# Kernel tuning notes

Hardware: AMD Instinct MI355X
Metric: run time of the kernel (lower is better)

The kernel has to match this reference:

```python
import jax, jax.numpy as jnp
import numpy as np

N, E, D, L, R = 100000, 500000, 128, 2, 10
EPS = 1e-5  # BatchNorm1d default eps


def setup_inputs() -> dict:
    key = jax.random.key(0)
    ks = jax.random.split(key, 10)
    return {
        "in_node_emb": jax.random.normal(ks[0], (N, D), jnp.float32),
        "in_rel_emb": jax.random.normal(ks[1], (R, D), jnp.float32),
        "w_in": jax.random.normal(ks[2], (L, D, D), jnp.float32) * 0.05,
        "w_out": jax.random.normal(ks[3], (L, D, D), jnp.float32) * 0.05,
        "w_loop": jax.random.normal(ks[4], (L, D, D), jnp.float32) * 0.05,
        "w_rel": jax.random.normal(ks[5], (L, D, D), jnp.float32) * 0.05,
        "loop_rel": jax.random.normal(ks[6], (L, 1, D), jnp.float32) * 0.05,
        "bias": jnp.zeros((L, D), jnp.float32),
        "edge_src": jax.random.randint(ks[7], (E,), 0, N),
        "edge_dst": jax.random.randint(ks[8], (E,), 0, N),
        "edge_type": jax.random.randint(ks[9], (E,), 0, R),
    }


def _gcn_forward(in_node_emb, in_rel_emb, w_in, w_out, w_loop, w_rel, loop_rel,
                 bias, edge_src, edge_dst, edge_type):
    x, r = in_node_emb, in_rel_emb
    ones_e = jnp.ones((E,), in_node_emb.dtype)
    for l in range(L):
        rel = jnp.concatenate([r, loop_rel[l]], axis=0)  # [R+1, D]; last row = self-loop relation
        rel_e = rel[edge_type]                            # [E, D] per-edge relation embedding

        def directed_msg(row, col, w):
            # gather -> compose ('mult') -> linear -> degree norm -> scatter-add at row
            comp = x[col] * rel_e                         # [E, D]
            m = comp @ w                                  # [E, D]
            deg = jnp.zeros((N,), x.dtype).at[row].add(ones_e)
            dinv = jnp.where(deg > 0, jax.lax.rsqrt(deg), 0.0)
            m = m * (dinv[row] * dinv[col])[:, None]
            return jnp.zeros((N, D), x.dtype).at[row].add(m)

        in_res = directed_msg(edge_src, edge_dst, w_in[l])   # original direction (src<-dst msgs)
        out_res = directed_msg(edge_dst, edge_src, w_out[l]) # mirrored direction
        loop_res = (x * loop_rel[l]) @ w_loop[l]             # self-loop (no norm)
        out = (in_res + out_res + loop_res) * (1.0 / 3.0) + bias[l]
        # BatchNorm1d over nodes, batch statistics, gamma=1 beta=0
        mean = out.mean(axis=0)
        var = out.var(axis=0)
        out = (out - mean) * jax.lax.rsqrt(var + EPS)
        x = jnp.tanh(out)
        r = (rel @ w_rel[l])[:-1]                            # transform rels, drop loop row
    return x, r


def reference(in_node_emb, in_rel_emb, w_in, w_out, w_loop, w_rel, loop_rel,
              bias, edge_src, edge_dst, edge_type):
    return _gcn_forward(in_node_emb, in_rel_emb, w_in, w_out, w_loop, w_rel,
                        loop_rel, bias, edge_src, edge_dst, edge_type)
```

## Files before the change

kernel.cpp:

```cpp
#include <hip/hip_runtime.h>
#include <math.h>

#define Nn 100000
#define Ee 500000
#define Dd 128
#define Rr 10
#define ND (Nn * Dd)
#define SCAN_CHUNK 1024
#define NBLK ((Nn + SCAN_CHUNK - 1) / SCAN_CHUNK)
#define LDK 136
#define EPSF 1e-5f

typedef _Float16 half_t;
typedef __attribute__((ext_vector_type(8))) _Float16 half8;
typedef __attribute__((ext_vector_type(4))) float f32x4;
typedef unsigned short ushort;
typedef unsigned int uint;
typedef unsigned long long u64;

union H2 { uint u; _Float16 h[2]; };
union H4 { u64 u; _Float16 h[4]; };
union H8 { uint4 q; _Float16 h[8]; };

__device__ __forceinline__ void atomAddF(float* p, float v) {
    unsafeAtomicAdd(p, v);
}

__global__ void kzeroi(int* p, int n) {
    int i = blockIdx.x * blockDim.x + threadIdx.x;
    int stride = gridDim.x * blockDim.x;
    for (; i < n; i += stride) p[i] = 0;
}

__global__ void khist(const int* __restrict__ src, const int* __restrict__ dst,
                      int* cnt_s, int* cnt_d, int ne) {
    int e = blockIdx.x * blockDim.x + threadIdx.x;
    if (e < ne) {
        atomicAdd(&cnt_s[src[e]], 1);
        atomicAdd(&cnt_d[dst[e]], 1);
    }
}

__global__ __launch_bounds__(256) void kscan1(
    const int* __restrict__ cnt_s, const int* __restrict__ cnt_d,
    int* off_s, int* off_d, int* bsum_s, int* bsum_d,
    float* dinv_s, float* dinv_d) {
    int dir = blockIdx.x >= NBLK;
    int lb = blockIdx.x - dir * NBLK;
    const int* cnt = dir ? cnt_d : cnt_s;
    int* off = dir ? off_d : off_s;
    int* bsum = dir ? bsum_d : bsum_s;
    float* dinv = dir ? dinv_d : dinv_s;
    __shared__ int s[256];
    int tid = threadIdx.x;
    int base = lb * SCAN_CHUNK + tid * 4;
    int v[4], sum = 0;
#pragma unroll
    for (int q = 0; q < 4; q++) {
        int c = (base + q < Nn) ? cnt[base + q] : 0;
        v[q] = c;
        sum += c;
        if (base + q < Nn) dinv[base + q] = (c > 0) ? rsqrtf((float)c) : 0.f;
    }
    s[tid] = sum;
    __syncthreads();
#pragma unroll
    for (int ofs = 1; ofs < 256; ofs <<= 1) {
        int t = (tid >= ofs) ? s[tid - ofs] : 0;
        __syncthreads();
        s[tid] += t;
        __syncthreads();
    }
    if (tid == 255) bsum[lb] = s[255];
    int run = s[tid] - sum;
#pragma unroll
    for (int q = 0; q < 4; q++) {
        if (base + q < Nn) off[base + q] = run;
        run += v[q];
    }
}

__global__ __launch_bounds__(128) void kscan2(int* bsum_s, int* bsum_d,
                                              int* off_s, int* off_d) {
    int dir = blockIdx.x;
    int* bsum = dir ? bsum_d : bsum_s;
    int* off = dir ? off_d : off_s;
    __shared__ int s[128];
    int tid = threadIdx.x;
    int v = (tid < NBLK) ? bsum[tid] : 0;
    s[tid] = v;
    __syncthreads();
#pragma unroll
    for (int ofs = 1; ofs < 128; ofs <<= 1) {
        int t = (tid >= ofs) ? s[tid - ofs] : 0;
        __syncthreads();
        s[tid] += t;
        __syncthreads();
    }
    if (tid < NBLK) bsum[tid] = s[tid] - v;
    if (tid == 127) off[Nn] = s[127];
}

__global__ void kscan3(int* off_s, int* off_d, const int* __restrict__ bsum_s,
                       const int* __restrict__ bsum_d, int* cur_s, int* cur_d) {
    int idx = blockIdx.x * blockDim.x + threadIdx.x;
    if (idx >= 2 * Nn) return;
    int dir = idx >= Nn;
    int i = idx - dir * Nn;
    int* off = dir ? off_d : off_s;
    const int* bsum = dir ? bsum_d : bsum_s;
    int* cur = dir ? cur_d : cur_s;
    int o = off[i] + bsum[i >> 10];
    off[i] = o;
    cur[i] = o;
}

__global__ void kscatter(const int* __restrict__ src, const int* __restrict__ dst,
                         const int* __restrict__ typ,
                         const float* __restrict__ dinv_s, const float* __restrict__ dinv_d,
                         int* cur_s, int* cur_d,
                         int* pack_s, float* norm_s, int* pack_d, float* norm_d, int ne) {
    int e = blockIdx.x * blockDim.x + threadIdx.x;
    if (e >= ne) return;
    int s = src[e], d = dst[e], t = typ[e];
    int ps = atomicAdd(&cur_s[s], 1);
    pack_s[ps] = (d << 4) | t;
    norm_s[ps] = dinv_s[s] * dinv_s[d];
    int pd = atomicAdd(&cur_d[d], 1);
    pack_d[pd] = (s << 4) | t;
    norm_d[pd] = dinv_d[d] * dinv_d[s];
}

__global__ __launch_bounds__(256) void kprep(
    const float* __restrict__ x, const float* __restrict__ lr0,
    const float* __restrict__ w_in, const float* __restrict__ w_out,
    const float* __restrict__ w_loop, const float* __restrict__ w_rel,
    const float* __restrict__ r0,
    half_t* __restrict__ xb, half_t* __restrict__ xlb,
    half_t* __restrict__ Wt, float* __restrict__ r1, float* __restrict__ r2) {
    int blk = blockIdx.x;
    int tid = threadIdx.x;
    if (blk < ND / 8 / 256) {
        int idx = blk * 256 + tid;
        int base = idx * 8;
        int k = base & 127;
        float4 v0 = *(const float4*)(x + base);
        float4 v1 = *(const float4*)(x + base + 4);
        float4 l0 = *(const float4*)(lr0 + k);
        float4 l1 = *(const float4*)(lr0 + k + 4);
        H8 xo, xl;
        xo.h[0] = (half_t)v0.x; xo.h[1] = (half_t)v0.y; xo.h[2] = (half_t)v0.z; xo.h[3] = (half_t)v0.w;
        xo.h[4] = (half_t)v1.x; xo.h[5] = (half_t)v1.y; xo.h[6] = (half_t)v1.z; xo.h[7] = (half_t)v1.w;
        xl.h[0] = (half_t)(v0.x * l0.x); xl.h[1] = (half_t)(v0.y * l0.y);
        xl.h[2] = (half_t)(v0.z * l0.z); xl.h[3] = (half_t)(v0.w * l0.w);
        xl.h[4] = (half_t)(v1.x * l1.x); xl.h[5] = (half_t)(v1.y * l1.y);
        xl.h[6] = (half_t)(v1.z * l1.z); xl.h[7] = (half_t)(v1.w * l1.w);
        *(uint4*)(xb + base) = xo.q;
        *(uint4*)(xlb + base) = xl.q;
    } else if (blk < ND / 8 / 256 + 384) {
        int idx = (blk - ND / 8 / 256) * 256 + tid;
        int l = idx >= 49152;
        int rem = idx - l * 49152;
        int p = rem >> 14, r2i = rem & 16383;
        int n = r2i >> 7, k = r2i & 127;
        const float* W = (p == 0) ? (w_in + l * 16384)
                       : ((p == 1) ? (w_out + l * 16384) : (w_loop + l * 16384));
        Wt[idx] = (half_t)W[k * 128 + n];
    } else {
        __shared__ float sr[Rr * Dd];
        for (int i = tid; i < Rr * Dd; i += 256) sr[i] = r0[i];
        __syncthreads();
        for (int ph = 0; ph < 2; ph++) {
            const float* w = w_rel + ph * 16384;
            float o[5];
#pragma unroll
            for (int q = 0; q < 5; q++) {
                int oi = tid + q * 256;
                int row = oi >> 7, j = oi & 127;
                float acc = 0.f;
                for (int k = 0; k < 128; k++) acc += sr[row * 128 + k] * w[k * 128 + j];
                o[q] = acc;
            }
            __syncthreads();
            float* dst = ph ? r2 : r1;
#pragma unroll
            for (int q = 0; q < 5; q++) {
                int oi = tid + q * 256;
                sr[oi] = o[q];
                dst[oi] = o[q];
            }
            __syncthreads();
        }
    }
}

__global__ __launch_bounds__(256) void kgather(
    const int* __restrict__ off_s, const int* __restrict__ pack_s, const float* __restrict__ nrm_s,
    const int* __restrict__ off_d, const int* __restrict__ pack_d, const float* __restrict__ nrm_d,
    const half_t* __restrict__ xb, const float* __restrict__ rel,
    half_t* __restrict__ aggin, half_t* __restrict__ aggout, int gb) {
    int blk = blockIdx.x;
    const int *off, *pack; const float* nrm; half_t* agg;
    if (blk < gb) { off = off_s; pack = pack_s; nrm = nrm_s; agg = aggin; }
    else { blk -= gb; off = off_d; pack = pack_d; nrm = nrm_d; agg = aggout; }
    int wv = threadIdx.x >> 6;
    int lane = threadIdx.x & 63;
    int half = lane >> 5;
    int hl = lane & 31;
    int node = blk * 8 + wv * 2 + half;
    bool valid = node < Nn;
    int nodec = valid ? node : (Nn - 1);
    int b = off[nodec];
    int e = off[nodec + 1];
    int n_it = valid ? (e - b) : 0;
    int other = __shfl(n_it, lane ^ 32, 64);
    int mx = n_it > other ? n_it : other;

    const u64* x4 = (const u64*)xb;
    const float4* r4 = (const float4*)rel;
    float a0 = 0.f, a1 = 0.f, a2 = 0.f, a3 = 0.f;

    int it = 0;
    for (; it + 1 < mx; it += 2) {
        bool c0 = it < n_it, c1 = it + 1 < n_it;
        int i0 = c0 ? (b + it) : 0;
        int i1 = c1 ? (b + it + 1) : 0;
        int p0 = pack[i0], p1 = pack[i1];
        float w0 = c0 ? nrm[i0] : 0.f;
        float w1 = c1 ? nrm[i1] : 0.f;
        H4 xv0, xv1;
        xv0.u = x4[(size_t)(p0 >> 4) * 32 + hl];
        xv1.u = x4[(size_t)(p1 >> 4) * 32 + hl];
        float4 rv0 = r4[(p0 & 15) * 32 + hl];
        float4 rv1 = r4[(p1 & 15) * 32 + hl];
        a0 += (float)xv0.h[0] * rv0.x * w0;
        a1 += (float)xv0.h[1] * rv0.y * w0;
        a2 += (float)xv0.h[2] * rv0.z * w0;
        a3 += (float)xv0.h[3] * rv0.w * w0;
        a0 += (float)xv1.h[0] * rv1.x * w1;
        a1 += (float)xv1.h[1] * rv1.y * w1;
        a2 += (float)xv1.h[2] * rv1.z * w1;
        a3 += (float)xv1.h[3] * rv1.w * w1;
    }
    if (it < mx) {
        bool c0 = it < n_it;
        int i0 = c0 ? (b + it) : 0;
        int p0 = pack[i0];
        float w0 = c0 ? nrm[i0] : 0.f;
        H4 xv0; xv0.u = x4[(size_t)(p0 >> 4) * 32 + hl];
        float4 rv0 = r4[(p0 & 15) * 32 + hl];
        a0 += (float)xv0.h[0] * rv0.x * w0;
        a1 += (float)xv0.h[1] * rv0.y * w0;
        a2 += (float)xv0.h[2] * rv0.z * w0;
        a3 += (float)xv0.h[3] * rv0.w * w0;
    }
    if (valid) {
        H4 o;
        o.h[0] = (half_t)a0; o.h[1] = (half_t)a1;
        o.h[2] = (half_t)a2; o.h[3] = (half_t)a3;
        ((u64*)agg)[(size_t)node * 32 + hl] = o.u;
    }
}

__global__ __launch_bounds__(256) void kmm(
    const half_t* __restrict__ aggin, const half_t* __restrict__ aggout,
    const half_t* __restrict__ xlb, const half_t* __restrict__ Wt,
    const float* __restrict__ bias, half_t* __restrict__ out,
    float* colsum, float* colsumsq) {
    __shared__ half_t sW[128 * LDK];
    const int tid = threadIdx.x;
    const int wv = tid >> 6;
    const int lane = tid & 63;
    const int col = lane & 15;
    const int quad = lane >> 4;
    const int m0 = blockIdx.x * 128;
    const int rowbase = m0 + wv * 32;

    f32x4 acc[2][8];
#pragma unroll
    for (int m = 0; m < 2; m++)
#pragma unroll
        for (int j = 0; j < 8; j++) acc[m][j] = (f32x4){0.f, 0.f, 0.f, 0.f};

    const half_t* Ap[3] = {aggin, aggout, xlb};
    int r0 = rowbase + col;
    int r1 = r0 + 16;
    int r0c = (r0 < Nn) ? r0 : (Nn - 1);
    int r1c = (r1 < Nn) ? r1 : (Nn - 1);

    for (int p = 0; p < 3; p++) {
        __syncthreads();
        {
            const half8* Wg = (const half8*)(Wt + p * 16384);
#pragma unroll
            for (int i = 0; i < 8; i++) {
                int c = tid + i * 256;
                int n = c >> 4, ko = (c & 15) * 8;
                *(half8*)(sW + n * LDK + ko) = Wg[c];
            }
        }
        __syncthreads();
        const half_t* A = Ap[p];
#pragma unroll
        for (int s = 0; s < 4; s++) {
            int ko = s * 32 + quad * 8;
            half8 va0 = *(const half8*)(A + r0c * Dd + ko);
            half8 va1 = *(const half8*)(A + r1c * Dd + ko);
#pragma unroll
            for (int j = 0; j < 8; j++) {
                half8 vb = *(const half8*)(sW + (j * 16 + col) * LDK + ko);
                acc[0][j] = __builtin_amdgcn_mfma_f32_16x16x32_f16(va0, vb, acc[0][j], 0, 0, 0);
                acc[1][j] = __builtin_amdgcn_mfma_f32_16x16x32_f16(va1, vb, acc[1][j], 0, 0, 0);
            }
        }
    }

    const float inv3 = 1.f / 3.f;
    float bcol[8], sum[8], ssq[8];
#pragma unroll
    for (int j = 0; j < 8; j++) {
        bcol[j] = bias[j * 16 + col];
        sum[j] = 0.f; ssq[j] = 0.f;
    }
#pragma unroll
    for (int m = 0; m < 2; m++) {
        int rb = rowbase + m * 16;
        if (rb < Nn) {
#pragma unroll
            for (int j = 0; j < 8; j++) {
#pragma unroll
                for (int r = 0; r < 4; r++) {
                    float v = acc[m][j][r] * inv3 + bcol[j];
                    out[(rb + quad * 4 + r) * Dd + j * 16 + col] = (half_t)v;
                    sum[j] += v;
                    ssq[j] += v * v;
                }
            }
        }
    }
#pragma unroll
    for (int j = 0; j < 8; j++) {
        sum[j] += __shfl_xor(sum[j], 16, 64);
        sum[j] += __shfl_xor(sum[j], 32, 64);
        ssq[j] += __shfl_xor(ssq[j], 16, 64);
        ssq[j] += __shfl_xor(ssq[j], 32, 64);
    }
    __syncthreads();
    float* sred = (float*)sW;
    if (quad == 0) {
#pragma unroll
        for (int j = 0; j < 8; j++) {
            sred[wv * 128 + j * 16 + col] = sum[j];
            sred[512 + wv * 128 + j * 16 + col] = ssq[j];
        }
    }
    __syncthreads();
    if (tid < 128) {
        float s = 0.f, s2 = 0.f;
#pragma unroll
        for (int w = 0; w < 4; w++) {
            s += sred[w * 128 + tid];
            s2 += sred[512 + w * 128 + tid];
        }
        atomAddF(&colsum[tid], s);
        atomAddF(&colsumsq[tid], s2);
    }
}

__global__ __launch_bounds__(256) void knorm0(const half_t* __restrict__ outh,
                                              const float* __restrict__ colsum,
                                              const float* __restrict__ colsumsq,
                                              const float* __restrict__ lr,
                                              half_t* __restrict__ xb,
                                              half_t* __restrict__ xlb) {
    __shared__ float sm[128], srs[128];
    int tid = threadIdx.x;
    if (tid < 128) {
        float m = colsum[tid] * (1.f / (float)Nn);
        float v = colsumsq[tid] * (1.f / (float)Nn) - m * m;
        sm[tid] = m;
        srs[tid] = rsqrtf(v + EPSF);
    }
    __syncthreads();
    int idx = blockIdx.x * 256 + tid;
    int base = idx * 8;
    int k = base & 127;
    H8 v; v.q = *(const uint4*)(outh + base);
    H8 xo, xl;
#pragma unroll
    for (int q = 0; q < 8; q++) {
        float t = tanhf(((float)v.h[q] - sm[k + q]) * srs[k + q]);
        xo.h[q] = (half_t)t;
        xl.h[q] = (half_t)(t * lr[k + q]);
    }
    *(uint4*)(xb + base) = xo.q;
    *(uint4*)(xlb + base) = xl.q;
}

__global__ __launch_bounds__(256) void knorm1(const half_t* __restrict__ outh,
                                              const float* __restrict__ colsum,
                                              const float* __restrict__ colsumsq,
                                              float* __restrict__ xn) {
    __shared__ float sm[128], srs[128];
    int tid = threadIdx.x;
    if (tid < 128) {
        float m = colsum[tid] * (1.f / (float)Nn);
        float v = colsumsq[tid] * (1.f / (float)Nn) - m * m;
        sm[tid] = m;
        srs[tid] = rsqrtf(v + EPSF);
    }
    __syncthreads();
    int idx = blockIdx.x * 256 + tid;
    int base = idx * 8;
    int k = base & 127;
    H8 v; v.q = *(const uint4*)(outh + base);
    float4 o0, o1;
    o0.x = tanhf(((float)v.h[0] - sm[k + 0]) * srs[k + 0]);
    o0.y = tanhf(((float)v.h[1] - sm[k + 1]) * srs[k + 1]);
    o0.z = tanhf(((float)v.h[2] - sm[k + 2]) * srs[k + 2]);
    o0.w = tanhf(((float)v.h[3] - sm[k + 3]) * srs[k + 3]);
    o1.x = tanhf(((float)v.h[4] - sm[k + 4]) * srs[k + 4]);
    o1.y = tanhf(((float)v.h[5] - sm[k + 5]) * srs[k + 5]);
    o1.z = tanhf(((float)v.h[6] - sm[k + 6]) * srs[k + 6]);
    o1.w = tanhf(((float)v.h[7] - sm[k + 7]) * srs[k + 7]);
    *(float4*)(xn + base) = o0;
    *(float4*)(xn + base + 4) = o1;
}

extern "C" void kernel_launch(void* const* d_in, const int* in_sizes, int n_in,
                              void* d_out, int out_size, void* d_ws, size_t ws_size,
                              hipStream_t stream) {
    const float* x0      = (const float*)d_in[0];
    const float* r0      = (const float*)d_in[1];
    const float* w_in    = (const float*)d_in[2];
    const float* w_out   = (const float*)d_in[3];
    const float* w_loop  = (const float*)d_in[4];
    const float* w_rel   = (const float*)d_in[5];
    const float* looprel = (const float*)d_in[6];
    const float* bias    = (const float*)d_in[7];
    const int* esrc = (const int*)d_in[8];
    const int* edst = (const int*)d_in[9];
    const int* etyp = (const int*)d_in[10];
    float* outp = (float*)d_out;

    half_t* us = (half_t*)d_ws;
    half_t* aggin_h  = us;
    half_t* aggout_h = us + (size_t)ND;
    half_t* xb       = us + 2 * (size_t)ND;
    half_t* xlb      = us + 3 * (size_t)ND;
    half_t* outh     = us + 4 * (size_t)ND;
    half_t* Wt       = us + 5 * (size_t)ND;
    float* fp = (float*)(us + 5 * (size_t)ND + 2 * 49152);
    float* dinv_s  = fp;   fp += Nn;
    float* dinv_d  = fp;   fp += Nn;
    float* r1      = fp;   fp += Rr * Dd;
    float* norm_s  = fp;   fp += Ee;
    float* norm_d  = fp;   fp += Ee;
    int* ip = (int*)fp;
    int* cnt_s  = ip;  ip += Nn;
    int* cnt_d  = ip;  ip += Nn;
    float* colsumA = (float*)ip;  ip += 2 * Dd;
    float* colsumB = (float*)ip;  ip += 2 * Dd;
    int* off_s  = ip;  ip += Nn + 1;
    int* off_d  = ip;  ip += Nn + 1;
    int* cur_s  = ip;  ip += Nn;
    int* cur_d  = ip;  ip += Nn;
    int* bsum_s = ip;  ip += 128;
    int* bsum_d = ip;  ip += 128;
    int* pack_s = ip;  ip += Ee;
    int* pack_d = ip;  ip += Ee;

    kzeroi<<<256, 256, 0, stream>>>(cnt_s, 2 * Nn + 4 * Dd);
    khist<<<(Ee + 255) / 256, 256, 0, stream>>>(esrc, edst, cnt_s, cnt_d, Ee);
    kscan1<<<2 * NBLK, 256, 0, stream>>>(cnt_s, cnt_d, off_s, off_d, bsum_s, bsum_d,
                                         dinv_s, dinv_d);
    kscan2<<<2, 128, 0, stream>>>(bsum_s, bsum_d, off_s, off_d);
    kscan3<<<(2 * Nn + 255) / 256, 256, 0, stream>>>(off_s, off_d, bsum_s, bsum_d,
                                                     cur_s, cur_d);
    kscatter<<<(Ee + 255) / 256, 256, 0, stream>>>(esrc, edst, etyp, dinv_s, dinv_d,
                                                   cur_s, cur_d, pack_s, norm_s,
                                                   pack_d, norm_d, Ee);
    kprep<<<ND / 8 / 256 + 384 + 1, 256, 0, stream>>>(
        x0, looprel, w_in, w_out, w_loop, w_rel, r0,
        xb, xlb, Wt, r1, outp + (size_t)ND);

    const int gb = (Nn + 7) / 8;
    for (int l = 0; l < 2; l++) {
        const float* rc = l ? r1 : r0;
        float* cs = l ? colsumB : colsumA;
        kgather<<<2 * gb, 256, 0, stream>>>(off_s, pack_s, norm_s, off_d, pack_d, norm_d,
                                            xb, rc, aggin_h, aggout_h, gb);
        kmm<<<(Nn + 127) / 128, 256, 0, stream>>>(aggin_h, aggout_h, xlb, Wt + l * 49152,
                                                  bias + l * Dd, outh, cs, cs + Dd);
        if (l == 0) {
            knorm0<<<ND / 8 / 256, 256, 0, stream>>>(outh, cs, cs + Dd, looprel + Dd, xb, xlb);
        } else {
            knorm1<<<ND / 8 / 256, 256, 0, stream>>>(outh, cs, cs + Dd, outp);
        }
    }
}
```

Baseline: 490.3 us.

## Pack edge index and norm into 64-bit records and unroll gather by eight

The scatter kernel now writes a single 64-bit record per edge that combines the packed neighbor/type index with the normalization weight, so the gather reads one array instead of two. The gather loop is restructured to load eight records, then eight x rows and relation rows, before accumulating, which exposes more memory-level parallelism. To make the unguarded over-read safe, the record arrays get 64 entries of padding and the relation tables are padded to 16 zeroed rows. The cost is more registers per thread and some wasted loads for nodes with few edges.

```diff
diff --git a/kernel.cpp b/kernel.cpp
--- a/kernel.cpp
+++ b/kernel.cpp
@@ -10,6 +10,7 @@
 #define NBLK ((Nn + SCAN_CHUNK - 1) / SCAN_CHUNK)
 #define LDK 136
 #define EPSF 1e-5f
+#define XBLK (ND / 8 / 256)
 
 typedef _Float16 half_t;
 typedef __attribute__((ext_vector_type(8))) _Float16 half8;
@@ -18,7 +19,6 @@
 typedef unsigned int uint;
 typedef unsigned long long u64;
 
-union H2 { uint u; _Float16 h[2]; };
 union H4 { u64 u; _Float16 h[4]; };
 union H8 { uint4 q; _Float16 h[8]; };
 
@@ -119,16 +119,16 @@
                          const int* __restrict__ typ,
                          const float* __restrict__ dinv_s, const float* __restrict__ dinv_d,
                          int* cur_s, int* cur_d,
-                         int* pack_s, float* norm_s, int* pack_d, float* norm_d, int ne) {
+                         u64* rec_s, u64* rec_d, int ne) {
     int e = blockIdx.x * blockDim.x + threadIdx.x;
     if (e >= ne) return;
     int s = src[e], d = dst[e], t = typ[e];
     int ps = atomicAdd(&cur_s[s], 1);
-    pack_s[ps] = (d << 4) | t;
-    norm_s[ps] = dinv_s[s] * dinv_s[d];
+    rec_s[ps] = (u64)(uint)((d << 4) | t) |
+                ((u64)__float_as_uint(dinv_s[s] * dinv_s[d]) << 32);
     int pd = atomicAdd(&cur_d[d], 1);
-    pack_d[pd] = (s << 4) | t;
-    norm_d[pd] = dinv_d[d] * dinv_d[s];
+    rec_d[pd] = (u64)(uint)((s << 4) | t) |
+                ((u64)__float_as_uint(dinv_d[d] * dinv_d[s]) << 32);
 }
 
 __global__ __launch_bounds__(256) void kprep(
@@ -137,10 +137,11 @@
     const float* __restrict__ w_loop, const float* __restrict__ w_rel,
     const float* __restrict__ r0,
     half_t* __restrict__ xb, half_t* __restrict__ xlb,
-    half_t* __restrict__ Wt, float* __restrict__ r1, float* __restrict__ r2) {
+    half_t* __restrict__ Wt, float* __restrict__ rel0p, float* __restrict__ rel1p,
+    float* __restrict__ r2out) {
     int blk = blockIdx.x;
     int tid = threadIdx.x;
-    if (blk < ND / 8 / 256) {
+    if (blk < XBLK) {
         int idx = blk * 256 + tid;
         int base = idx * 8;
         int k = base & 127;
@@ -157,16 +158,16 @@
         xl.h[6] = (half_t)(v1.z * l1.z); xl.h[7] = (half_t)(v1.w * l1.w);
         *(uint4*)(xb + base) = xo.q;
         *(uint4*)(xlb + base) = xl.q;
-    } else if (blk < ND / 8 / 256 + 384) {
-        int idx = (blk - ND / 8 / 256) * 256 + tid;
+    } else if (blk < XBLK + 384) {
+        int idx = (blk - XBLK) * 256 + tid;
         int l = idx >= 49152;
         int rem = idx - l * 49152;
-        int p = rem >> 14, r2i = rem & 16383;
-        int n = r2i >> 7, k = r2i & 127;
+        int p = rem >> 14, ri = rem & 16383;
+        int n = ri >> 7, k = ri & 127;
         const float* W = (p == 0) ? (w_in + l * 16384)
                        : ((p == 1) ? (w_out + l * 16384) : (w_loop + l * 16384));
         Wt[idx] = (half_t)W[k * 128 + n];
-    } else {
+    } else if (blk == XBLK + 384) {
         __shared__ float sr[Rr * Dd];
         for (int i = tid; i < Rr * Dd; i += 256) sr[i] = r0[i];
         __syncthreads();
@@ -182,7 +183,7 @@
                 o[q] = acc;
             }
             __syncthreads();
-            float* dst = ph ? r2 : r1;
+            float* dst = ph ? r2out : rel1p;
 #pragma unroll
             for (int q = 0; q < 5; q++) {
                 int oi = tid + q * 256;
@@ -191,23 +192,26 @@
             }
             __syncthreads();
         }
+        for (int i = Rr * Dd + tid; i < 16 * Dd; i += 256) rel1p[i] = 0.f;
+    } else {
+        for (int i = tid; i < 16 * Dd; i += 256) rel0p[i] = (i < Rr * Dd) ? r0[i] : 0.f;
     }
 }
 
 __global__ __launch_bounds__(256) void kgather(
-    const int* __restrict__ off_s, const int* __restrict__ pack_s, const float* __restrict__ nrm_s,
-    const int* __restrict__ off_d, const int* __restrict__ pack_d, const float* __restrict__ nrm_d,
-    const half_t* __restrict__ xb, const float* __restrict__ rel,
+    const int* __restrict__ off_s, const u64* __restrict__ rec_s,
+    const int* __restrict__ off_d, const u64* __restrict__ rec_d,
+    const half_t* __restrict__ xb, const float* __restrict__ relp,
     half_t* __restrict__ aggin, half_t* __restrict__ aggout, int gb) {
     int blk = blockIdx.x;
-    const int *off, *pack; const float* nrm; half_t* agg;
-    if (blk < gb) { off = off_s; pack = pack_s; nrm = nrm_s; agg = aggin; }
-    else { blk -= gb; off = off_d; pack = pack_d; nrm = nrm_d; agg = aggout; }
+    const int* off; const u64* rec; half_t* agg;
+    if (blk < gb) { off = off_s; rec = rec_s; agg = aggin; }
+    else { blk -= gb; off = off_d; rec = rec_d; agg = aggout; }
     int wv = threadIdx.x >> 6;
     int lane = threadIdx.x & 63;
-    int half = lane >> 5;
+    int hf = lane >> 5;
     int hl = lane & 31;
-    int node = blk * 8 + wv * 2 + half;
+    int node = blk * 8 + wv * 2 + hf;
     bool valid = node < Nn;
     int nodec = valid ? node : (Nn - 1);
     int b = off[nodec];
@@ -217,42 +221,31 @@
     int mx = n_it > other ? n_it : other;
 
     const u64* x4 = (const u64*)xb;
-    const float4* r4 = (const float4*)rel;
+    const float4* r4 = (const float4*)relp;
     float a0 = 0.f, a1 = 0.f, a2 = 0.f, a3 = 0.f;
 
-    int it = 0;
-    for (; it + 1 < mx; it += 2) {
-        bool c0 = it < n_it, c1 = it + 1 < n_it;
-        int i0 = c0 ? (b + it) : 0;
-        int i1 = c1 ? (b + it + 1) : 0;
-        int p0 = pack[i0], p1 = pack[i1];
-        float w0 = c0 ? nrm[i0] : 0.f;
-        float w1 = c1 ? nrm[i1] : 0.f;
-        H4 xv0, xv1;
-        xv0.u = x4[(size_t)(p0 >> 4) * 32 + hl];
-        xv1.u = x4[(size_t)(p1 >> 4) * 32 + hl];
-        float4 rv0 = r4[(p0 & 15) * 32 + hl];
-        float4 rv1 = r4[(p1 & 15) * 32 + hl];
-        a0 += (float)xv0.h[0] * rv0.x * w0;
-        a1 += (float)xv0.h[1] * rv0.y * w0;
-        a2 += (float)xv0.h[2] * rv0.z * w0;
-        a3 += (float)xv0.h[3] * rv0.w * w0;
-        a0 += (float)xv1.h[0] * rv1.x * w1;
-        a1 += (float)xv1.h[1] * rv1.y * w1;
-        a2 += (float)xv1.h[2] * rv1.z * w1;
-        a3 += (float)xv1.h[3] * rv1.w * w1;
-    }
-    if (it < mx) {
-        bool c0 = it < n_it;
-        int i0 = c0 ? (b + it) : 0;
-        int p0 = pack[i0];
-        float w0 = c0 ? nrm[i0] : 0.f;
-        H4 xv0; xv0.u = x4[(size_t)(p0 >> 4) * 32 + hl];
-        float4 rv0 = r4[(p0 & 15) * 32 + hl];
-        a0 += (float)xv0.h[0] * rv0.x * w0;
-        a1 += (float)xv0.h[1] * rv0.y * w0;
-        a2 += (float)xv0.h[2] * rv0.z * w0;
-        a3 += (float)xv0.h[3] * rv0.w * w0;
+    for (int it0 = 0; it0 < mx; it0 += 8) {
+        u64 rr[8];
+#pragma unroll
+        for (int q = 0; q < 8; q++) rr[q] = rec[b + it0 + q];
+        H4 xv[8]; float4 rl[8]; float wq[8];
+#pragma unroll
+        for (int q = 0; q < 8; q++) {
+            uint p = (uint)rr[q];
+            uint nmb = (uint)(rr[q] >> 32);
+            bool c = (it0 + q) < n_it;
+            wq[q] = c ? __uint_as_float(nmb) : 0.f;
+            int xi = c ? (int)(p >> 4) : 0;
+            xv[q].u = x4[(size_t)xi * 32 + hl];
+            rl[q] = r4[(p & 15u) * 32 + hl];
+        }
+#pragma unroll
+        for (int q = 0; q < 8; q++) {
+            a0 += (float)xv[q].h[0] * rl[q].x * wq[q];
+            a1 += (float)xv[q].h[1] * rl[q].y * wq[q];
+            a2 += (float)xv[q].h[2] * rl[q].z * wq[q];
+            a3 += (float)xv[q].h[3] * rl[q].w * wq[q];
+        }
     }
     if (valid) {
         H4 o;
@@ -450,12 +443,13 @@
     half_t* xlb      = us + 3 * (size_t)ND;
     half_t* outh     = us + 4 * (size_t)ND;
     half_t* Wt       = us + 5 * (size_t)ND;
-    float* fp = (float*)(us + 5 * (size_t)ND + 2 * 49152);
+    u64* rec_s = (u64*)(us + 5 * (size_t)ND + 2 * 49152);
+    u64* rec_d = rec_s + (Ee + 64);
+    float* fp = (float*)(rec_d + (Ee + 64));
     float* dinv_s  = fp;   fp += Nn;
     float* dinv_d  = fp;   fp += Nn;
-    float* r1      = fp;   fp += Rr * Dd;
-    float* norm_s  = fp;   fp += Ee;
-    float* norm_d  = fp;   fp += Ee;
+    float* rel0p   = fp;   fp += 16 * Dd;
+    float* rel1p   = fp;   fp += 16 * Dd;
     int* ip = (int*)fp;
     int* cnt_s  = ip;  ip += Nn;
     int* cnt_d  = ip;  ip += Nn;
@@ -467,8 +461,6 @@
     int* cur_d  = ip;  ip += Nn;
     int* bsum_s = ip;  ip += 128;
     int* bsum_d = ip;  ip += 128;
-    int* pack_s = ip;  ip += Ee;
-    int* pack_d = ip;  ip += Ee;
 
     kzeroi<<<256, 256, 0, stream>>>(cnt_s, 2 * Nn + 4 * Dd);
     khist<<<(Ee + 255) / 256, 256, 0, stream>>>(esrc, edst, cnt_s, cnt_d, Ee);
@@ -478,18 +470,17 @@
     kscan3<<<(2 * Nn + 255) / 256, 256, 0, stream>>>(off_s, off_d, bsum_s, bsum_d,
                                                      cur_s, cur_d);
     kscatter<<<(Ee + 255) / 256, 256, 0, stream>>>(esrc, edst, etyp, dinv_s, dinv_d,
-                                                   cur_s, cur_d, pack_s, norm_s,
-                                                   pack_d, norm_d, Ee);
-    kprep<<<ND / 8 / 256 + 384 + 1, 256, 0, stream>>>(
+                                                   cur_s, cur_d, rec_s, rec_d, Ee);
+    kprep<<<XBLK + 384 + 2, 256, 0, stream>>>(
         x0, looprel, w_in, w_out, w_loop, w_rel, r0,
-        xb, xlb, Wt, r1, outp + (size_t)ND);
+        xb, xlb, Wt, rel0p, rel1p, outp + (size_t)ND);
 
     const int gb = (Nn + 7) / 8;
     for (int l = 0; l < 2; l++) {
-        const float* rc = l ? r1 : r0;
+        const float* relp = l ? rel1p : rel0p;
         float* cs = l ? colsumB : colsumA;
-        kgather<<<2 * gb, 256, 0, stream>>>(off_s, pack_s, norm_s, off_d, pack_d, norm_d,
-                                            xb, rc, aggin_h, aggout_h, gb);
+        kgather<<<2 * gb, 256, 0, stream>>>(off_s, rec_s, off_d, rec_d,
+                                            xb, relp, aggin_h, aggout_h, gb);
         kmm<<<(Nn + 127) / 128, 256, 0, stream>>>(aggin_h, aggout_h, xlb, Wt + l * 49152,
                                                   bias + l * Dd, outh, cs, cs + Dd);
         if (l == 0) {
```

Result: slower. 509.5 us (+3.9%).
